# Kernel optimization log

Hardware: AMD Instinct MI355X
Metric: run time of the kernel (lower is better)

Reference implementation:

```python
import jax, jax.numpy as jnp
import numpy as np

B, TT, TA, H = 2, 128, 512, 1024
EPS = 1e-5


def _conv1d(x, w, b, pad):
    # x: [B, C_in, T], w: [C_out, C_in, K] -> [B, C_out, T]
    y = jax.lax.conv_general_dilated(x, w, window_strides=(1,), padding=[(pad, pad)],
                                     dimension_numbers=('NCH', 'OIH', 'NCH'))
    return y + b[None, :, None]


def _groupnorm1(x, g, b):
    # GroupNorm(num_groups=1): normalize over (C, T) per sample. x: [B, C, T]
    mu = jnp.mean(x, axis=(1, 2), keepdims=True)
    var = jnp.var(x, axis=(1, 2), keepdims=True)
    xn = (x - mu) * jax.lax.rsqrt(var + EPS)
    return xn * g[None, :, None] + b[None, :, None]


def setup_inputs() -> dict:
    key = jax.random.key(0)
    ks = jax.random.split(key, 16)
    s = 0.02
    return {
        'text_hidden': jax.random.normal(ks[0], (B, TT, H), jnp.float32),
        'audio_hidden': jax.random.normal(ks[1], (B, TA, H), jnp.float32),
        # alignment_proj: Linear(2H, H) -> ReLU -> Linear(H, 1)
        'a_w1': jax.random.normal(ks[2], (2 * H, H), jnp.float32) * s,
        'a_b1': jnp.zeros((H,), jnp.float32),
        'a_w2': jax.random.normal(ks[3], (H, 1), jnp.float32) * s,
        'a_b2': jnp.zeros((1,), jnp.float32),
        # duration_predictor: Conv1d(H,H,3) ReLU GN(1,H) Conv1d(H,H,3) ReLU GN(1,H) Conv1d(H,1,1)
        'd_w1': jax.random.normal(ks[4], (H, H, 3), jnp.float32) * s,
        'd_b1': jnp.zeros((H,), jnp.float32),
        'gn1_g': jnp.ones((H,), jnp.float32),
        'gn1_b': jnp.zeros((H,), jnp.float32),
        'd_w2': jax.random.normal(ks[5], (H, H, 3), jnp.float32) * s,
        'd_b2': jnp.zeros((H,), jnp.float32),
        'gn2_g': jnp.ones((H,), jnp.float32),
        'gn2_b': jnp.zeros((H,), jnp.float32),
        'd_w3': jax.random.normal(ks[6], (1, H, 1), jnp.float32) * s,
        'd_b3': jnp.zeros((1,), jnp.float32),
    }


def reference(text_hidden, audio_hidden, a_w1, a_b1, a_w2, a_b2,
              d_w1, d_b1, gn1_g, gn1_b, d_w2, d_b2, gn2_g, gn2_b, d_w3, d_b3):
    # ---- predict_durations ----
    x = jnp.swapaxes(text_hidden, 1, 2)                      # [B, H, TT]
    x = _groupnorm1(jax.nn.relu(_conv1d(x, d_w1, d_b1, 1)), gn1_g, gn1_b)
    x = _groupnorm1(jax.nn.relu(_conv1d(x, d_w2, d_b2, 1)), gn2_g, gn2_b)
    x = _conv1d(x, d_w3, d_b3, 0)                            # [B, 1, TT]
    durations = jax.nn.softplus(x[:, 0, :])                  # [B, TT]

    # ---- soft_mas (temperature = 1.0) ----
    # Linear on concat([text, audio]) == text @ W1[:H] + audio @ W1[H:] + b1
    t_part = jnp.einsum('bth,hd->btd', text_hidden, a_w1[:H])    # [B, TT, H]
    a_part = jnp.einsum('bah,hd->bad', audio_hidden, a_w1[H:])   # [B, TA, H]
    hid = jax.nn.relu(t_part[:, :, None, :] + a_part[:, None, :, :] + a_b1)  # [B,TT,TA,H]
    logits = jnp.einsum('btad,do->bta', hid, a_w2) + a_b2[0]     # [B, TT, TA]

    pos = jnp.arange(TA, dtype=logits.dtype)                     # audio positions j
    expected = jnp.arange(TT, dtype=logits.dtype) * (TA / TT)    # expected pos per text i
    monotonic_bias = -0.1 * jnp.abs(pos[None, :] - expected[:, None])  # [TT, TA]
    logits = logits + monotonic_bias[None, :, :]

    alignment = jax.nn.softmax(logits, axis=-1)
    return alignment, durations
```

## Files before the change

kernel.cpp:

```cpp
#include <hip/hip_runtime.h>
#include <hip/hip_bf16.h>


typedef __bf16 bf16_t;
typedef __bf16 bf16x8 __attribute__((ext_vector_type(8)));
typedef __bf16 bf16x4 __attribute__((ext_vector_type(4)));
typedef float  f32x4  __attribute__((ext_vector_type(4)));
typedef _Float16 f16_t;
typedef _Float16 f16x2 __attribute__((ext_vector_type(2)));
typedef _Float16 f16x4 __attribute__((ext_vector_type(4)));
typedef int v4i __attribute__((ext_vector_type(4)));

#define EPSV 1e-5f

#define GLD(dst, ptr, off) \
    asm volatile("global_load_dwordx4 %0, %1, off offset:%c2" \
                 : "=v"(dst) : "v"(ptr), "n"(off) : "memory")
#define WAITV(n) do { \
    asm volatile("s_waitcnt vmcnt(%c0)" :: "n"(n) : "memory"); \
    __builtin_amdgcn_sched_barrier(0); } while (0)

__device__ __forceinline__ bf16x8 as_bf16x8(v4i v) {
    union { v4i i; bf16x8 h; } u; u.i = v; return u.h;
}

#define OFF_TEXTP    0u
#define OFF_AUDIOP   524288u
#define OFF_W1TOP    2621440u
#define OFF_W1BOT    4718592u
#define OFF_WC1      6815744u
#define OFF_WC2      13107200u
#define OFF_TP       19398656u
#define OFF_W2F      19922944u
#define OFF_APT      20447232u
#define OFF_XP0      22544384u
#define OFF_XP1      23076864u
#define OFF_Y2       23609344u
#define OFF_BST1     24133632u
#define OFF_BST2     24137728u
#define OFF_LP       24141824u
#define OFF_SG       26238976u
#define OFF_SB       26251264u
#define OFF_SGF      26263552u
#define OFF_SBF      26267648u

__global__ __launch_bounds__(256) void prep_k(
    const float* __restrict__ text, const float* __restrict__ audio,
    const float* __restrict__ w1,
    const float* __restrict__ w1c, const float* __restrict__ w2c,
    const float* __restrict__ w2,
    const float* __restrict__ g1, const float* __restrict__ b1g,
    bf16_t* __restrict__ textP, bf16_t* __restrict__ xp0,
    bf16_t* __restrict__ audioP,
    bf16_t* __restrict__ topP, bf16_t* __restrict__ botP,
    bf16_t* __restrict__ wc1, bf16_t* __restrict__ wc2,
    bf16_t* __restrict__ xp1, f16_t* __restrict__ w2f,
    float* __restrict__ Sg, float* __restrict__ Sb,
    float* __restrict__ SgF, float* __restrict__ SbF)
{
    __shared__ float tile[32][33];
    const int bid = blockIdx.x;
    if (bid < 1280) {
        const int e = (bid * 256 + threadIdx.x) * 4;
        if (e < 262144) {
            float4 v = *(const float4*)&text[e];
            bf16x4 o; o[0] = (bf16_t)v.x; o[1] = (bf16_t)v.y; o[2] = (bf16_t)v.z; o[3] = (bf16_t)v.w;
            const int bt = e >> 10, h = e & 1023;
            const int b = bt >> 7, t = bt & 127;
            *(bf16x4*)&xp0[(size_t)(b * 130 + 1 + t) * 1024 + h] = o;
            const int lane = (bt & 15) | (((h >> 3) & 3) << 4);
            *(bf16x4*)&textP[((size_t)((bt >> 4) * 32 + (h >> 5))) * 512 + lane * 8 + (h & 7)] = o;
        } else {
            const int ea = e - 262144;
            float4 v = *(const float4*)&audio[ea];
            bf16x4 o; o[0] = (bf16_t)v.x; o[1] = (bf16_t)v.y; o[2] = (bf16_t)v.z; o[3] = (bf16_t)v.w;
            const int ba = ea >> 10, h = ea & 1023;
            const int lane = (ba & 15) | (((h >> 3) & 3) << 4);
            *(bf16x4*)&audioP[((size_t)((ba >> 4) * 32 + (h >> 5))) * 512 + lane * 8 + (h & 7)] = o;
        }
    } else if (bid < 3328) {
        const int b2 = bid - 1280;
        const int bx = b2 & 31, by = b2 >> 5;
        const int tx = threadIdx.x & 31, ty = threadIdx.x >> 5;
        #pragma unroll
        for (int j = 0; j < 4; ++j)
            tile[ty + j * 8][tx] = w1[(size_t)(by * 32 + ty + j * 8) * 1024 + bx * 32 + tx];
        __syncthreads();
        if (threadIdx.x < 128) {
            const int rbl = threadIdx.x >> 6, lane = threadIdx.x & 63;
            const int dl = rbl * 16 + (lane & 15);
            const int lkp = lane >> 4;
            bf16x8 v8;
            #pragma unroll
            for (int e2 = 0; e2 < 8; ++e2) v8[e2] = (bf16_t)tile[lkp * 8 + e2][dl];
            const int d = bx * 32 + dl;
            bf16_t* out = (by < 32) ? topP : botP;
            *(bf16x8*)&out[((size_t)((d >> 4) * 32 + (by & 31))) * 512 + lane * 8] = v8;
        }
    } else if (bid < 5376) {
        int b2 = bid - 3328;
        const int is2 = (b2 >= 1024) ? 1 : 0;
        const float* w = is2 ? w2c : w1c;
        bf16_t* wc = is2 ? wc2 : wc1;
        b2 &= 1023;
        const int o = b2, i4 = threadIdx.x;
        const float* src = w + (size_t)o * 3072 + i4 * 12;
        float4 v0 = *(const float4*)&src[0];
        float4 v1 = *(const float4*)&src[4];
        float4 v2 = *(const float4*)&src[8];
        const float f[12] = {v0.x, v0.y, v0.z, v0.w, v1.x, v1.y, v1.z, v1.w, v2.x, v2.y, v2.z, v2.w};
        float g4[4] = {1.f, 1.f, 1.f, 1.f}, bb4[4] = {0.f, 0.f, 0.f, 0.f};
        if (is2) {
            float4 gv = *(const float4*)&g1[i4 * 4];
            float4 bv = *(const float4*)&b1g[i4 * 4];
            g4[0] = gv.x; g4[1] = gv.y; g4[2] = gv.z; g4[3] = gv.w;
            bb4[0] = bv.x; bb4[1] = bv.y; bb4[2] = bv.z; bb4[3] = bv.w;
        }
        const int i0 = i4 * 4;
        const int lane = (o & 15) | (((i0 >> 3) & 3) << 4);
        float sgr[3] = {0.f, 0.f, 0.f}, sbr[3] = {0.f, 0.f, 0.f};
        #pragma unroll
        for (int r = 0; r < 3; ++r) {
            bf16x4 o4;
            #pragma unroll
            for (int j = 0; j < 4; ++j) {
                const float wv = f[j * 3 + r];
                const float ws = wv * g4[j];
                sgr[r] += ws;
                sbr[r] += wv * bb4[j];
                o4[j] = (bf16_t)(is2 ? ws : wv);
            }
            *(bf16x4*)&wc[((size_t)(r * 2048 + (o >> 4) * 32 + (i0 >> 5))) * 512 + lane * 8 + (i0 & 7)] = o4;
        }
        if (is2) {
            #pragma unroll
            for (int off = 32; off > 0; off >>= 1) {
                #pragma unroll
                for (int r = 0; r < 3; ++r) {
                    sgr[r] += __shfl_xor(sgr[r], off);
                    sbr[r] += __shfl_xor(sbr[r], off);
                }
            }
            float* red = &tile[0][0];
            const int wid = threadIdx.x >> 6, lane2 = threadIdx.x & 63;
            if (lane2 == 0) {
                #pragma unroll
                for (int r = 0; r < 3; ++r) {
                    red[wid * 6 + r] = sgr[r];
                    red[wid * 6 + 3 + r] = sbr[r];
                }
            }
            __syncthreads();
            if (threadIdx.x < 6) {
                const float v = red[threadIdx.x] + red[6 + threadIdx.x]
                              + red[12 + threadIdx.x] + red[18 + threadIdx.x];
                if (threadIdx.x < 3) Sg[o * 3 + threadIdx.x] = v;
                else                 Sb[o * 3 + threadIdx.x - 3] = v;
                red[24 + threadIdx.x] = v;
            }
            __syncthreads();
            if (threadIdx.x == 0)      SgF[o] = red[24] + red[25] + red[26];
            else if (threadIdx.x == 1) SbF[o] = red[27] + red[28] + red[29];
        }
    } else {
        const int tid = threadIdx.x;
        const int rowmap[4] = {0, 129, 130, 259};
        const int f = tid * 16;
        const int r = f >> 10, w = f & 1023;
        bf16x8 z8 = (bf16x8)(bf16_t)0.0f;
        bf16_t* p0 = xp0 + (size_t)rowmap[r] * 1024 + w;
        bf16_t* p1 = xp1 + (size_t)rowmap[r] * 1024 + w;
        *(bf16x8*)p0 = z8; *(bf16x8*)(p0 + 8) = z8;
        *(bf16x8*)p1 = z8; *(bf16x8*)(p1 + 8) = z8;
        float4 wv = *(const float4*)&w2[tid * 4];
        f16x4 wo; wo[0] = (f16_t)wv.x; wo[1] = (f16_t)wv.y; wo[2] = (f16_t)wv.z; wo[3] = (f16_t)wv.w;
        *(f16x4*)&w2f[tid * 4] = wo;
    }
}

__device__ __forceinline__ float wave_red_add(float v) {
    #pragma unroll
    for (int off = 32; off > 0; off >>= 1) v += __shfl_xor(v, off);
    return v;
}

__device__ __forceinline__ void conv_body(
    const bf16_t* __restrict__ WcP, const bf16_t* __restrict__ xp,
    int by, int b, int tbase, int w, int l, bf16_t* Bs, int tid,
    f32x4& acc0, f32x4& acc1)
{
    const int lm = l & 15, lk = (l >> 4) * 8;
    const bf16_t* xrow = xp + (size_t)(b * 130 + tbase) * 1024;
    #pragma unroll 1
    for (int c = 0; c < 4; ++c) {
        __syncthreads();
        for (int idx = tid; idx < 1088; idx += 512) {
            const int row = idx >> 5, col = (idx & 31) * 8;
            *(v4i*)&Bs[row * 264 + col] =
                *(const v4i*)&xrow[(size_t)row * 1024 + c * 256 + col];
        }
        __syncthreads();
        const int kc = c * 8 + w;
        const bf16_t* a0 = WcP + ((size_t)(by * 32 + kc)) * 512 + l * 8;
        v4i A0, A1, A2;
        GLD(A0, a0, 0);
        GLD(A1, a0 + 1048576, 0);
        GLD(A2, a0 + 2097152, 0);
        const int cb = w * 32 + lk;
        bf16x8 b00 = *(const bf16x8*)&Bs[(lm + 0) * 264 + cb];
        bf16x8 b10 = *(const bf16x8*)&Bs[(lm + 16) * 264 + cb];
        bf16x8 b01 = *(const bf16x8*)&Bs[(lm + 1) * 264 + cb];
        bf16x8 b11 = *(const bf16x8*)&Bs[(lm + 17) * 264 + cb];
        bf16x8 b02 = *(const bf16x8*)&Bs[(lm + 2) * 264 + cb];
        bf16x8 b12 = *(const bf16x8*)&Bs[(lm + 18) * 264 + cb];
        WAITV(2);
        acc0 = __builtin_amdgcn_mfma_f32_16x16x32_bf16(as_bf16x8(A0), b00, acc0, 0, 0, 0);
        acc1 = __builtin_amdgcn_mfma_f32_16x16x32_bf16(as_bf16x8(A0), b10, acc1, 0, 0, 0);
        WAITV(1);
        acc0 = __builtin_amdgcn_mfma_f32_16x16x32_bf16(as_bf16x8(A1), b01, acc0, 0, 0, 0);
        acc1 = __builtin_amdgcn_mfma_f32_16x16x32_bf16(as_bf16x8(A1), b11, acc1, 0, 0, 0);
        WAITV(0);
        acc0 = __builtin_amdgcn_mfma_f32_16x16x32_bf16(as_bf16x8(A2), b02, acc0, 0, 0, 0);
        acc1 = __builtin_amdgcn_mfma_f32_16x16x32_bf16(as_bf16x8(A2), b12, acc1, 0, 0, 0);
    }
    __syncthreads();
}

__global__ __launch_bounds__(512) void p2_k(
    const bf16_t* __restrict__ wc1, const bf16_t* __restrict__ xp0,
    const float* __restrict__ d_b1, bf16_t* __restrict__ xp1,
    float* __restrict__ bstat1,
    const bf16_t* __restrict__ textP, const bf16_t* __restrict__ topP,
    const float* __restrict__ a_b1, f16_t* __restrict__ tp,
    const bf16_t* __restrict__ audioP, const bf16_t* __restrict__ botP,
    f16_t* __restrict__ apT4)
{
    __shared__ float smem[8448];
    __shared__ float sred[8], sredq[8];
    const int bid = blockIdx.x;
    const int tid = threadIdx.x;
    const int w = tid >> 6, l = tid & 63;
    const int lm = l & 15, lh = l >> 4;
    if (bid < 512) {
        const int bx = bid >> 6, by = bid & 63;
        const int bt0 = bx * 32, m0 = by * 16;
        const int b = bt0 >> 7, tbase = bt0 & 127;
        f32x4 acc0 = (f32x4)(0.0f), acc1 = (f32x4)(0.0f);
        conv_body(wc1, xp0, by, b, tbase, w, l, (bf16_t*)smem, tid, acc0, acc1);
        float* sl = smem + w * 528;
        #pragma unroll
        for (int r = 0; r < 4; ++r) {
            sl[(lh * 4 + r) * 33 + lm] = acc0[r];
            sl[(lh * 4 + r) * 33 + 16 + lm] = acc1[r];
        }
        __syncthreads();
        const int mm = tid >> 5, nn = tid & 31;
        float v = 0.f;
        #pragma unroll
        for (int ww = 0; ww < 8; ++ww) v += smem[ww * 528 + mm * 33 + nn];
        v = fmaxf(v + d_b1[m0 + mm], 0.f);
        float s = wave_red_add(v), q = wave_red_add(v * v);
        if (l == 0) { sred[w] = s; sredq[w] = q; }
        xp1[(size_t)(b * 130 + 1 + tbase + nn) * 1024 + m0 + mm] = (bf16_t)v;
        __syncthreads();
        if (tid == 0) {
            float ts = 0.f, tq = 0.f;
            #pragma unroll
            for (int ww = 0; ww < 8; ++ww) { ts += sred[ww]; tq += sredq[ww]; }
            bstat1[bid * 2] = ts; bstat1[bid * 2 + 1] = tq;
        }
    } else {
        const bf16_t *At, *Bm;
        int d0, r0, is_tp;
        if (bid < 768) {
            const int unit = bid - 512;
            d0 = (unit & 31) * 32; r0 = (unit >> 5) * 32;
            At = topP; Bm = textP; is_tp = 1;
        } else {
            const int unit = bid - 768;
            d0 = (unit & 31) * 32; r0 = (unit >> 5) * 32;
            At = botP; Bm = audioP; is_tp = 0;
        }
        const int rb0 = d0 >> 4, rbB = r0 >> 4;
        const bf16_t* Ap0 = At + ((size_t)(rb0 * 32 + w * 4)) * 512 + l * 8;
        const bf16_t* Ap1 = Ap0 + 16384;
        const bf16_t* Bp0 = Bm + ((size_t)(rbB * 32 + w * 4)) * 512 + l * 8;
        const bf16_t* Bp1 = Bp0 + 16384;
        v4i qa0[4], qa1[4], qb0[4], qb1[4];
        GLD(qa0[0], Ap0,    0); GLD(qa1[0], Ap1,    0); GLD(qb0[0], Bp0,    0); GLD(qb1[0], Bp1,    0);
        GLD(qa0[1], Ap0, 1024); GLD(qa1[1], Ap1, 1024); GLD(qb0[1], Bp0, 1024); GLD(qb1[1], Bp1, 1024);
        GLD(qa0[2], Ap0, 2048); GLD(qa1[2], Ap1, 2048); GLD(qb0[2], Bp0, 2048); GLD(qb1[2], Bp1, 2048);
        GLD(qa0[3], Ap0, 3072); GLD(qa1[3], Ap1, 3072); GLD(qb0[3], Bp0, 3072); GLD(qb1[3], Bp1, 3072);
        f32x4 acc[2][2];
        #pragma unroll
        for (int mt = 0; mt < 2; ++mt)
            #pragma unroll
            for (int nt = 0; nt < 2; ++nt) acc[mt][nt] = (f32x4)(0.0f);
#define GMF(cc, n) \
        WAITV(n); \
        acc[0][0] = __builtin_amdgcn_mfma_f32_16x16x32_bf16(as_bf16x8(qa0[cc]), as_bf16x8(qb0[cc]), acc[0][0], 0, 0, 0); \
        acc[0][1] = __builtin_amdgcn_mfma_f32_16x16x32_bf16(as_bf16x8(qa0[cc]), as_bf16x8(qb1[cc]), acc[0][1], 0, 0, 0); \
        acc[1][0] = __builtin_amdgcn_mfma_f32_16x16x32_bf16(as_bf16x8(qa1[cc]), as_bf16x8(qb0[cc]), acc[1][0], 0, 0, 0); \
        acc[1][1] = __builtin_amdgcn_mfma_f32_16x16x32_bf16(as_bf16x8(qa1[cc]), as_bf16x8(qb1[cc]), acc[1][1], 0, 0, 0)
        GMF(0, 12); GMF(1, 8); GMF(2, 4); GMF(3, 0);
#undef GMF
        float* sl = smem + w * 1056;
        #pragma unroll
        for (int mt = 0; mt < 2; ++mt)
            #pragma unroll
            for (int nt = 0; nt < 2; ++nt)
                #pragma unroll
                for (int r = 0; r < 4; ++r)
                    sl[(mt * 16 + lh * 4 + r) * 33 + nt * 16 + lm] = acc[mt][nt][r];
        __syncthreads();
        const int m = tid >> 4, n2 = (tid & 15) * 2;
        float v0 = 0.f, v1 = 0.f;
        #pragma unroll
        for (int ww = 0; ww < 8; ++ww) {
            v0 += smem[ww * 1056 + m * 33 + n2];
            v1 += smem[ww * 1056 + m * 33 + n2 + 1];
        }
        if (is_tp) {
            const float bb = a_b1[d0 + m];
            tp[(size_t)(r0 + n2) * 1024 + d0 + m] = (f16_t)(v0 + bb);
            tp[(size_t)(r0 + n2 + 1) * 1024 + d0 + m] = (f16_t)(v1 + bb);
        } else {
            const int h = d0 + m, hq = h >> 2, hr = h & 3;
            const int a0 = r0 + n2;
            const int bbk = a0 >> 9, al = a0 & 511;
            apT4[((size_t)hq * 1024 + bbk * 512 + al) * 4 + hr] = (f16_t)v0;
            apT4[((size_t)hq * 1024 + bbk * 512 + al + 1) * 4 + hr] = (f16_t)v1;
        }
    }
}

__device__ __forceinline__ void reduce_bstat(
    const float* __restrict__ bstat, int b, int tid,
    float* sr, float* sq, float& mu, float& rsig)
{
    const int lane = tid & 63, wid = tid >> 6;
    float s = 0.f, q = 0.f;
    if (tid < 256) {
        float2 v = ((const float2*)bstat)[b * 256 + tid];
        s = v.x; q = v.y;
    }
    #pragma unroll
    for (int off = 32; off > 0; off >>= 1) {
        s += __shfl_xor(s, off);
        q += __shfl_xor(q, off);
    }
    if (lane == 0) { sr[wid] = s; sq[wid] = q; }
    __syncthreads();
    float ts = 0.f, tq = 0.f;
    #pragma unroll
    for (int i = 0; i < 8; ++i) { ts += sr[i]; tq += sq[i]; }
    const float cnt = 131072.f;
    mu = ts / cnt;
    const float var = tq / cnt - mu * mu;
    rsig = rsqrtf(var + EPSV);
}

__device__ __forceinline__ float dot2_acc(f16x2 x, f16x2 w, float acc) {
#if __has_builtin(__builtin_amdgcn_fdot2)
    return __builtin_amdgcn_fdot2(x, w, acc, false);
#else
    return acc + (float)x[0] * (float)w[0] + (float)x[1] * (float)w[1];
#endif
}

__global__ __launch_bounds__(512) void p3_k(
    const bf16_t* __restrict__ wc2, const bf16_t* __restrict__ xp1,
    const float* __restrict__ d_b2, bf16_t* __restrict__ y2,
    float* __restrict__ bstat2, const float* __restrict__ bstat1,
    const float* __restrict__ SgF, const float* __restrict__ SbF,
    const float* __restrict__ Sg3, const float* __restrict__ Sb3,
    const f16_t* __restrict__ tp, const f16_t* __restrict__ apT4,
    const f16_t* __restrict__ w2f, float* __restrict__ lp)
{
    __shared__ float smem[4608];
    __shared__ float sred[8], sredq[8], sr[8], sq[8];
    const int bid = blockIdx.x;
    const int tid = threadIdx.x;
    if (bid < 512) {
        const int w = tid >> 6, l = tid & 63;
        const int lm = l & 15, lh = l >> 4;
        const int bx = bid >> 6, by = bid & 63;
        const int bt0 = bx * 32, m0 = by * 16;
        const int b = bt0 >> 7, tbase = bt0 & 127;
        f32x4 acc0 = (f32x4)(0.0f), acc1 = (f32x4)(0.0f);
        conv_body(wc2, xp1, by, b, tbase, w, l, (bf16_t*)smem, tid, acc0, acc1);
        float* sl = smem + w * 528;
        #pragma unroll
        for (int r = 0; r < 4; ++r) {
            sl[(lh * 4 + r) * 33 + lm] = acc0[r];
            sl[(lh * 4 + r) * 33 + 16 + lm] = acc1[r];
        }
        __syncthreads();
        const int mm = tid >> 5, nn = tid & 31;
        float vraw = 0.f;
        #pragma unroll
        for (int ww = 0; ww < 8; ++ww) vraw += smem[ww * 528 + mm * 33 + nn];
        float mu, rsig;
        reduce_bstat(bstat1, b, tid, sr, sq, mu, rsig);
        const int o = m0 + mm, tloc = tbase + nn;
        float sg = SgF[o], sb = SbF[o];
        if (tloc == 0)   { sg -= Sg3[o * 3];     sb -= Sb3[o * 3]; }
        if (tloc == 127) { sg -= Sg3[o * 3 + 2]; sb -= Sb3[o * 3 + 2]; }
        float v = fmaxf(rsig * vraw + sb - mu * rsig * sg + d_b2[o], 0.f);
        float s = wave_red_add(v), q = wave_red_add(v * v);
        if ((tid & 63) == 0) { sred[tid >> 6] = s; sredq[tid >> 6] = q; }
        y2[(size_t)(b * 128 + tloc) * 1024 + o] = (bf16_t)v;
        __syncthreads();
        if (tid == 0) {
            float ts = 0.f, tq = 0.f;
            #pragma unroll
            for (int ww = 0; ww < 8; ++ww) { ts += sred[ww]; tq += sredq[ww]; }
            bstat2[bid * 2] = ts; bstat2[bid * 2 + 1] = tq;
        }
    } else {
        const int lb = bid - 512;
        const int hc = lb >> 6, btp = lb & 63;
        const int bt0 = btp * 4;
        const int b = bt0 >> 7;
        const int a = tid;
        const f16_t* tpr = tp + (size_t)bt0 * 1024 + hc * 256;
        const f16_t* w2r = w2f + hc * 256;
        const f16_t* apc = apT4 + ((size_t)(hc * 64) * 1024 + b * 512 + a) * 4;
        float acc[4] = {0.f, 0.f, 0.f, 0.f};
        const f16x2 zero = (f16x2)(f16_t)0.0f;
#define L_A0(i) (*(const f16x4*)(apc + (size_t)(2 * (i)) * 4096))
#define L_A1(i) (*(const f16x4*)(apc + (size_t)(2 * (i) + 1) * 4096))
        constexpr int PF = 4;
        f16x4 pa[PF], pb[PF];
        #pragma unroll
        for (int i = 0; i < PF; ++i) { pa[i] = L_A0(i); pb[i] = L_A1(i); }
        #pragma unroll
        for (int i = 0; i < 32; ++i) {
            const int sl = i % PF;
            const int hq = 2 * i;
            f16x4 a0 = pa[sl], a1 = pb[sl];
            f16x4 w0 = *(const f16x4*)&w2r[hq * 4];
            f16x4 w1 = *(const f16x4*)&w2r[hq * 4 + 4];
            #pragma unroll
            for (int r = 0; r < 4; ++r) {
                f16x4 t0 = *(const f16x4*)&tpr[r * 1024 + hq * 4];
                f16x4 t1 = *(const f16x4*)&tpr[r * 1024 + hq * 4 + 4];
                f16x2 p;
                p = __builtin_elementwise_max((f16x2){t0[0] + a0[0], t0[1] + a0[1]}, zero);
                acc[r] = dot2_acc(p, (f16x2){w0[0], w0[1]}, acc[r]);
                p = __builtin_elementwise_max((f16x2){t0[2] + a0[2], t0[3] + a0[3]}, zero);
                acc[r] = dot2_acc(p, (f16x2){w0[2], w0[3]}, acc[r]);
                p = __builtin_elementwise_max((f16x2){t1[0] + a1[0], t1[1] + a1[1]}, zero);
                acc[r] = dot2_acc(p, (f16x2){w1[0], w1[1]}, acc[r]);
                p = __builtin_elementwise_max((f16x2){t1[2] + a1[2], t1[3] + a1[3]}, zero);
                acc[r] = dot2_acc(p, (f16x2){w1[2], w1[3]}, acc[r]);
            }
            const int nx = i + PF;
            if (nx < 32) { pa[sl] = L_A0(nx); pb[sl] = L_A1(nx); }
        }
#undef L_A0
#undef L_A1
        float* dst = lp + (size_t)(hc * 256 + bt0) * 512 + a;
        #pragma unroll
        for (int r = 0; r < 4; ++r) dst[(size_t)r * 512] = acc[r];
    }
}

__global__ __launch_bounds__(512) void combine_k(
    const float* __restrict__ lp, const float* __restrict__ b2,
    const bf16_t* __restrict__ y2, const float* __restrict__ bstat2,
    const float* __restrict__ g, const float* __restrict__ bet,
    const float* __restrict__ w3, const float* __restrict__ b3,
    float* __restrict__ out)
{
    __shared__ float redm[8], redsum[8];
    const int bid = blockIdx.x;
    const int tid = threadIdx.x;
    if (bid < 256) {
        const int bt = bid, t = bt & 127;
        const int a = tid;
        const int lane = a & 63, wid = a >> 6;
        const size_t base = (size_t)bt * 512 + a;
        float v = lp[base] + lp[131072 + base] + lp[262144 + base] + lp[393216 + base];
        v += b2[0] - 0.1f * fabsf((float)a - 4.0f * (float)t);
        float m = v;
        #pragma unroll
        for (int off = 32; off > 0; off >>= 1) m = fmaxf(m, __shfl_xor(m, off));
        if (lane == 0) redm[wid] = m;
        __syncthreads();
        float M = redm[0];
        #pragma unroll
        for (int i = 1; i < 8; ++i) M = fmaxf(M, redm[i]);
        const float e = expf(v - M);
        float s = e;
        #pragma unroll
        for (int off = 32; off > 0; off >>= 1) s += __shfl_xor(s, off);
        if (lane == 0) redsum[wid] = s;
        __syncthreads();
        float S = redsum[0];
        #pragma unroll
        for (int i = 1; i < 8; ++i) S += redsum[i];
        out[(size_t)bt * 512 + a] = e * (1.0f / S);
    } else {
        const int cb = bid - 256;
        const int b = (cb * 8) >> 7;
        float mu, rsig;
        reduce_bstat(bstat2, b, tid, redm, redsum, mu, rsig);
        const int lane = tid & 63, w = tid >> 6;
        const int bt = cb * 8 + w;
        const bf16_t* row = y2 + (size_t)bt * 1024 + lane * 16;
        float s1 = 0.f, s2 = 0.f, s3 = 0.f;
        #pragma unroll
        for (int c = 0; c < 2; ++c) {
            bf16x8 yv = *(const bf16x8*)(row + c * 8);
            #pragma unroll
            for (int j = 0; j < 8; ++j) {
                const int i = lane * 16 + c * 8 + j;
                const float gw = g[i] * w3[i];
                s1 += gw * (float)yv[j];
                s2 += gw;
                s3 += bet[i] * w3[i];
            }
        }
        #pragma unroll
        for (int off = 32; off > 0; off >>= 1) {
            s1 += __shfl_xor(s1, off);
            s2 += __shfl_xor(s2, off);
            s3 += __shfl_xor(s3, off);
        }
        if (lane == 0) {
            const float t = rsig * (s1 - mu * s2) + s3 + b3[0];
            out[131072 + bt] = fmaxf(t, 0.f) + log1pf(expf(-fabsf(t)));
        }
    }
}

extern "C" void kernel_launch(void* const* d_in, const int* in_sizes, int n_in,
                              void* d_out, int out_size, void* d_ws, size_t ws_size,
                              hipStream_t stream) {
    const float* text   = (const float*)d_in[0];
    const float* audio  = (const float*)d_in[1];
    const float* a_w1   = (const float*)d_in[2];
    const float* a_b1   = (const float*)d_in[3];
    const float* a_w2   = (const float*)d_in[4];
    const float* a_b2   = (const float*)d_in[5];
    const float* d_w1   = (const float*)d_in[6];
    const float* d_b1   = (const float*)d_in[7];
    const float* gn1_g  = (const float*)d_in[8];
    const float* gn1_b  = (const float*)d_in[9];
    const float* d_w2   = (const float*)d_in[10];
    const float* d_b2   = (const float*)d_in[11];
    const float* gn2_g  = (const float*)d_in[12];
    const float* gn2_b  = (const float*)d_in[13];
    const float* d_w3   = (const float*)d_in[14];
    const float* d_b3   = (const float*)d_in[15];

    char* ws = (char*)d_ws;
    float* outf = (float*)d_out;

    bf16_t* textP    = (bf16_t*)(ws + OFF_TEXTP);
    bf16_t* audioP   = (bf16_t*)(ws + OFF_AUDIOP);
    bf16_t* topP     = (bf16_t*)(ws + OFF_W1TOP);
    bf16_t* botP     = (bf16_t*)(ws + OFF_W1BOT);
    bf16_t* wc1      = (bf16_t*)(ws + OFF_WC1);
    bf16_t* wc2      = (bf16_t*)(ws + OFF_WC2);
    f16_t*  tp       = (f16_t*) (ws + OFF_TP);
    f16_t*  w2f      = (f16_t*) (ws + OFF_W2F);
    f16_t*  apT4     = (f16_t*) (ws + OFF_APT);
    bf16_t* xp0      = (bf16_t*)(ws + OFF_XP0);
    bf16_t* xp1      = (bf16_t*)(ws + OFF_XP1);
    bf16_t* y2       = (bf16_t*)(ws + OFF_Y2);
    float*  bstat1   = (float*) (ws + OFF_BST1);
    float*  bstat2   = (float*) (ws + OFF_BST2);
    float*  lp       = (float*) (ws + OFF_LP);
    float*  Sg3      = (float*) (ws + OFF_SG);
    float*  Sb3      = (float*) (ws + OFF_SB);
    float*  SgFp     = (float*) (ws + OFF_SGF);
    float*  SbFp     = (float*) (ws + OFF_SBF);

    prep_k<<<dim3(5377), 256, 0, stream>>>(text, audio, a_w1, d_w1, d_w2, a_w2,
                                           gn1_g, gn1_b,
                                           textP, xp0, audioP, topP, botP,
                                           wc1, wc2, xp1, w2f, Sg3, Sb3,
                                           SgFp, SbFp);
    p2_k<<<dim3(1792), 512, 0, stream>>>(wc1, xp0, d_b1, xp1, bstat1,
                                         textP, topP, a_b1, tp,
                                         audioP, botP, apT4);
    p3_k<<<dim3(768), 512, 0, stream>>>(wc2, xp1, d_b2, y2, bstat2, bstat1,
                                        SgFp, SbFp, Sg3, Sb3, tp, apT4, w2f, lp);
    combine_k<<<dim3(288), 512, 0, stream>>>(lp, a_b2, y2, bstat2,
                                             gn2_g, gn2_b, d_w3, d_b3, outf);
}
```

Before: 152.8 us.

## Move conv2 weight prep into p2 kernel, pair stores, prefetch A before LDS fill

The conv2 weight repacking and GroupNorm-folding sums move out of the prep kernel into extra blocks of the second kernel, so this work runs alongside the conv1 and projection GEMMs and the prep kernel shrinks. Packed bf16 stores are merged into 16-byte writes by exchanging halves between adjacent lanes. In the conv loop, the global A-fragment loads are now issued before the shared-memory tile fill, which hides their latency. The trade-off is a larger p2 grid, where the extra blocks compete with the GEMM blocks for compute units.

```diff
diff --git a/kernel.cpp b/kernel.cpp
--- a/kernel.cpp
+++ b/kernel.cpp
@@ -22,6 +22,17 @@
 
 __device__ __forceinline__ bf16x8 as_bf16x8(v4i v) {
     union { v4i i; bf16x8 h; } u; u.i = v; return u.h;
+}
+
+__device__ __forceinline__ void pair_store16(bf16_t* even_addr, bf16x4 v, int t) {
+    union { bf16x4 h; unsigned u[2]; } a; a.h = v;
+    const unsigned ox = __shfl_down(a.u[0], 1);
+    const unsigned oy = __shfl_down(a.u[1], 1);
+    if (!(t & 1)) {
+        union { unsigned u[4]; v4i i; } o;
+        o.u[0] = a.u[0]; o.u[1] = a.u[1]; o.u[2] = ox; o.u[3] = oy;
+        *(v4i*)even_addr = o.i;
+    }
 }
 
 #define OFF_TEXTP    0u
@@ -47,47 +58,48 @@
 __global__ __launch_bounds__(256) void prep_k(
     const float* __restrict__ text, const float* __restrict__ audio,
     const float* __restrict__ w1,
-    const float* __restrict__ w1c, const float* __restrict__ w2c,
-    const float* __restrict__ w2,
-    const float* __restrict__ g1, const float* __restrict__ b1g,
+    const float* __restrict__ w1c, const float* __restrict__ w2,
     bf16_t* __restrict__ textP, bf16_t* __restrict__ xp0,
     bf16_t* __restrict__ audioP,
     bf16_t* __restrict__ topP, bf16_t* __restrict__ botP,
-    bf16_t* __restrict__ wc1, bf16_t* __restrict__ wc2,
-    bf16_t* __restrict__ xp1, f16_t* __restrict__ w2f,
-    float* __restrict__ Sg, float* __restrict__ Sb,
-    float* __restrict__ SgF, float* __restrict__ SbF)
+    bf16_t* __restrict__ wc1,
+    bf16_t* __restrict__ xp1, f16_t* __restrict__ w2f)
 {
     __shared__ float tile[32][33];
     const int bid = blockIdx.x;
+    const int tid = threadIdx.x;
     if (bid < 1280) {
-        const int e = (bid * 256 + threadIdx.x) * 4;
+        const int e = (bid * 256 + tid) * 4;
         if (e < 262144) {
             float4 v = *(const float4*)&text[e];
             bf16x4 o; o[0] = (bf16_t)v.x; o[1] = (bf16_t)v.y; o[2] = (bf16_t)v.z; o[3] = (bf16_t)v.w;
             const int bt = e >> 10, h = e & 1023;
             const int b = bt >> 7, t = bt & 127;
             *(bf16x4*)&xp0[(size_t)(b * 130 + 1 + t) * 1024 + h] = o;
-            const int lane = (bt & 15) | (((h >> 3) & 3) << 4);
-            *(bf16x4*)&textP[((size_t)((bt >> 4) * 32 + (h >> 5))) * 512 + lane * 8 + (h & 7)] = o;
+            const int h0 = h & ~7;
+            const int lane = (bt & 15) | (((h0 >> 3) & 3) << 4);
+            bf16_t* ea = &textP[((size_t)((bt >> 4) * 32 + (h0 >> 5))) * 512 + lane * 8];
+            pair_store16(ea, o, tid);
         } else {
-            const int ea = e - 262144;
-            float4 v = *(const float4*)&audio[ea];
+            const int ea4 = e - 262144;
+            float4 v = *(const float4*)&audio[ea4];
             bf16x4 o; o[0] = (bf16_t)v.x; o[1] = (bf16_t)v.y; o[2] = (bf16_t)v.z; o[3] = (bf16_t)v.w;
-            const int ba = ea >> 10, h = ea & 1023;
-            const int lane = (ba & 15) | (((h >> 3) & 3) << 4);
-            *(bf16x4*)&audioP[((size_t)((ba >> 4) * 32 + (h >> 5))) * 512 + lane * 8 + (h & 7)] = o;
+            const int ba = ea4 >> 10, h = ea4 & 1023;
+            const int h0 = h & ~7;
+            const int lane = (ba & 15) | (((h0 >> 3) & 3) << 4);
+            bf16_t* ea = &audioP[((size_t)((ba >> 4) * 32 + (h0 >> 5))) * 512 + lane * 8];
+            pair_store16(ea, o, tid);
         }
     } else if (bid < 3328) {
         const int b2 = bid - 1280;
         const int bx = b2 & 31, by = b2 >> 5;
-        const int tx = threadIdx.x & 31, ty = threadIdx.x >> 5;
+        const int tx = tid & 31, ty = tid >> 5;
         #pragma unroll
         for (int j = 0; j < 4; ++j)
             tile[ty + j * 8][tx] = w1[(size_t)(by * 32 + ty + j * 8) * 1024 + bx * 32 + tx];
         __syncthreads();
-        if (threadIdx.x < 128) {
-            const int rbl = threadIdx.x >> 6, lane = threadIdx.x & 63;
+        if (tid < 128) {
+            const int rbl = tid >> 6, lane = tid & 63;
             const int dl = rbl * 16 + (lane & 15);
             const int lkp = lane >> 4;
             bf16x8 v8;
@@ -97,73 +109,25 @@
             bf16_t* out = (by < 32) ? topP : botP;
             *(bf16x8*)&out[((size_t)((d >> 4) * 32 + (by & 31))) * 512 + lane * 8] = v8;
         }
-    } else if (bid < 5376) {
-        int b2 = bid - 3328;
-        const int is2 = (b2 >= 1024) ? 1 : 0;
-        const float* w = is2 ? w2c : w1c;
-        bf16_t* wc = is2 ? wc2 : wc1;
-        b2 &= 1023;
-        const int o = b2, i4 = threadIdx.x;
-        const float* src = w + (size_t)o * 3072 + i4 * 12;
+    } else if (bid < 4352) {
+        const int o = bid - 3328;
+        const int i0 = tid * 4;
+        const float* src = w1c + (size_t)o * 3072 + tid * 12;
         float4 v0 = *(const float4*)&src[0];
         float4 v1 = *(const float4*)&src[4];
         float4 v2 = *(const float4*)&src[8];
         const float f[12] = {v0.x, v0.y, v0.z, v0.w, v1.x, v1.y, v1.z, v1.w, v2.x, v2.y, v2.z, v2.w};
-        float g4[4] = {1.f, 1.f, 1.f, 1.f}, bb4[4] = {0.f, 0.f, 0.f, 0.f};
-        if (is2) {
-            float4 gv = *(const float4*)&g1[i4 * 4];
-            float4 bv = *(const float4*)&b1g[i4 * 4];
-            g4[0] = gv.x; g4[1] = gv.y; g4[2] = gv.z; g4[3] = gv.w;
-            bb4[0] = bv.x; bb4[1] = bv.y; bb4[2] = bv.z; bb4[3] = bv.w;
-        }
-        const int i0 = i4 * 4;
-        const int lane = (o & 15) | (((i0 >> 3) & 3) << 4);
-        float sgr[3] = {0.f, 0.f, 0.f}, sbr[3] = {0.f, 0.f, 0.f};
+        const int ip = i0 & ~7;
+        const int lane = (o & 15) | (((ip >> 3) & 3) << 4);
         #pragma unroll
         for (int r = 0; r < 3; ++r) {
             bf16x4 o4;
             #pragma unroll
-            for (int j = 0; j < 4; ++j) {
-                const float wv = f[j * 3 + r];
-                const float ws = wv * g4[j];
-                sgr[r] += ws;
-                sbr[r] += wv * bb4[j];
-                o4[j] = (bf16_t)(is2 ? ws : wv);
-            }
-            *(bf16x4*)&wc[((size_t)(r * 2048 + (o >> 4) * 32 + (i0 >> 5))) * 512 + lane * 8 + (i0 & 7)] = o4;
-        }
-        if (is2) {
-            #pragma unroll
-            for (int off = 32; off > 0; off >>= 1) {
-                #pragma unroll
-                for (int r = 0; r < 3; ++r) {
-                    sgr[r] += __shfl_xor(sgr[r], off);
-                    sbr[r] += __shfl_xor(sbr[r], off);
-                }
-            }
-            float* red = &tile[0][0];
-            const int wid = threadIdx.x >> 6, lane2 = threadIdx.x & 63;
-            if (lane2 == 0) {
-                #pragma unroll
-                for (int r = 0; r < 3; ++r) {
-                    red[wid * 6 + r] = sgr[r];
-                    red[wid * 6 + 3 + r] = sbr[r];
-                }
-            }
-            __syncthreads();
-            if (threadIdx.x < 6) {
-                const float v = red[threadIdx.x] + red[6 + threadIdx.x]
-                              + red[12 + threadIdx.x] + red[18 + threadIdx.x];
-                if (threadIdx.x < 3) Sg[o * 3 + threadIdx.x] = v;
-                else                 Sb[o * 3 + threadIdx.x - 3] = v;
-                red[24 + threadIdx.x] = v;
-            }
-            __syncthreads();
-            if (threadIdx.x == 0)      SgF[o] = red[24] + red[25] + red[26];
-            else if (threadIdx.x == 1) SbF[o] = red[27] + red[28] + red[29];
+            for (int j = 0; j < 4; ++j) o4[j] = (bf16_t)f[j * 3 + r];
+            bf16_t* ea = &wc1[((size_t)(r * 2048 + (o >> 4) * 32 + (ip >> 5))) * 512 + lane * 8];
+            pair_store16(ea, o4, tid);
         }
     } else {
-        const int tid = threadIdx.x;
         const int rowmap[4] = {0, 129, 130, 259};
         const int f = tid * 16;
         const int r = f >> 10, w = f & 1023;
@@ -194,18 +158,18 @@
     #pragma unroll 1
     for (int c = 0; c < 4; ++c) {
         __syncthreads();
-        for (int idx = tid; idx < 1088; idx += 512) {
-            const int row = idx >> 5, col = (idx & 31) * 8;
-            *(v4i*)&Bs[row * 264 + col] =
-                *(const v4i*)&xrow[(size_t)row * 1024 + c * 256 + col];
-        }
-        __syncthreads();
         const int kc = c * 8 + w;
         const bf16_t* a0 = WcP + ((size_t)(by * 32 + kc)) * 512 + l * 8;
         v4i A0, A1, A2;
         GLD(A0, a0, 0);
         GLD(A1, a0 + 1048576, 0);
         GLD(A2, a0 + 2097152, 0);
+        for (int idx = tid; idx < 1088; idx += 512) {
+            const int row = idx >> 5, col = (idx & 31) * 8;
+            *(v4i*)&Bs[row * 264 + col] =
+                *(const v4i*)&xrow[(size_t)row * 1024 + c * 256 + col];
+        }
+        __syncthreads();
         const int cb = w * 32 + lk;
         bf16x8 b00 = *(const bf16x8*)&Bs[(lm + 0) * 264 + cb];
         bf16x8 b10 = *(const bf16x8*)&Bs[(lm + 16) * 264 + cb];
@@ -233,7 +197,11 @@
     const bf16_t* __restrict__ textP, const bf16_t* __restrict__ topP,
     const float* __restrict__ a_b1, f16_t* __restrict__ tp,
     const bf16_t* __restrict__ audioP, const bf16_t* __restrict__ botP,
-    f16_t* __restrict__ apT4)
+    f16_t* __restrict__ apT4,
+    const float* __restrict__ w2c, const float* __restrict__ g1,
+    const float* __restrict__ b1g, bf16_t* __restrict__ wc2,
+    float* __restrict__ Sg3, float* __restrict__ Sb3,
+    float* __restrict__ SgF, float* __restrict__ SbF)
 {
     __shared__ float smem[8448];
     __shared__ float sred[8], sredq[8];
@@ -269,7 +237,7 @@
             for (int ww = 0; ww < 8; ++ww) { ts += sred[ww]; tq += sredq[ww]; }
             bstat1[bid * 2] = ts; bstat1[bid * 2 + 1] = tq;
         }
-    } else {
+    } else if (bid < 1792) {
         const bf16_t *At, *Bm;
         int d0, r0, is_tp;
         if (bid < 768) {
@@ -331,6 +299,63 @@
             apT4[((size_t)hq * 1024 + bbk * 512 + al) * 4 + hr] = (f16_t)v0;
             apT4[((size_t)hq * 1024 + bbk * 512 + al + 1) * 4 + hr] = (f16_t)v1;
         }
+    } else {
+        const int half = tid >> 8, t = tid & 255;
+        const int o = (bid - 1792) * 2 + half;
+        const int i0 = t * 4;
+        const float* src = w2c + (size_t)o * 3072 + t * 12;
+        float4 v0 = *(const float4*)&src[0];
+        float4 v1 = *(const float4*)&src[4];
+        float4 v2 = *(const float4*)&src[8];
+        const float f[12] = {v0.x, v0.y, v0.z, v0.w, v1.x, v1.y, v1.z, v1.w, v2.x, v2.y, v2.z, v2.w};
+        float4 gv = *(const float4*)&g1[i0];
+        float4 bv = *(const float4*)&b1g[i0];
+        const float g4[4] = {gv.x, gv.y, gv.z, gv.w};
+        const float bb4[4] = {bv.x, bv.y, bv.z, bv.w};
+        const int ip = i0 & ~7;
+        const int lane = (o & 15) | (((ip >> 3) & 3) << 4);
+        float sgr[3] = {0.f, 0.f, 0.f}, sbr[3] = {0.f, 0.f, 0.f};
+        #pragma unroll
+        for (int r = 0; r < 3; ++r) {
+            bf16x4 o4;
+            #pragma unroll
+            for (int j = 0; j < 4; ++j) {
+                const float wv = f[j * 3 + r];
+                const float ws = wv * g4[j];
+                sgr[r] += ws;
+                sbr[r] += wv * bb4[j];
+                o4[j] = (bf16_t)ws;
+            }
+            bf16_t* ea = &wc2[((size_t)(r * 2048 + (o >> 4) * 32 + (ip >> 5))) * 512 + lane * 8];
+            pair_store16(ea, o4, t);
+        }
+        #pragma unroll
+        for (int off = 32; off > 0; off >>= 1) {
+            #pragma unroll
+            for (int r = 0; r < 3; ++r) {
+                sgr[r] += __shfl_xor(sgr[r], off);
+                sbr[r] += __shfl_xor(sbr[r], off);
+            }
+        }
+        float* red = smem + half * 32;
+        const int wid = t >> 6, lane2 = t & 63;
+        if (lane2 == 0) {
+            #pragma unroll
+            for (int r = 0; r < 3; ++r) {
+                red[wid * 6 + r] = sgr[r];
+                red[wid * 6 + 3 + r] = sbr[r];
+            }
+        }
+        __syncthreads();
+        if (t < 6) {
+            const float v = red[t] + red[6 + t] + red[12 + t] + red[18 + t];
+            if (t < 3) Sg3[o * 3 + t] = v;
+            else       Sb3[o * 3 + t - 3] = v;
+            red[24 + t] = v;
+        }
+        __syncthreads();
+        if (t == 0)      SgF[o] = red[24] + red[25] + red[26];
+        else if (t == 1) SbF[o] = red[27] + red[28] + red[29];
     }
 }
 
@@ -578,14 +603,14 @@
     float*  SgFp     = (float*) (ws + OFF_SGF);
     float*  SbFp     = (float*) (ws + OFF_SBF);
 
-    prep_k<<<dim3(5377), 256, 0, stream>>>(text, audio, a_w1, d_w1, d_w2, a_w2,
-                                           gn1_g, gn1_b,
+    prep_k<<<dim3(4353), 256, 0, stream>>>(text, audio, a_w1, d_w1, a_w2,
                                            textP, xp0, audioP, topP, botP,
-                                           wc1, wc2, xp1, w2f, Sg3, Sb3,
-                                           SgFp, SbFp);
-    p2_k<<<dim3(1792), 512, 0, stream>>>(wc1, xp0, d_b1, xp1, bstat1,
+                                           wc1, xp1, w2f);
+    p2_k<<<dim3(2304), 512, 0, stream>>>(wc1, xp0, d_b1, xp1, bstat1,
                                          textP, topP, a_b1, tp,
-                                         audioP, botP, apT4);
+                                         audioP, botP, apT4,
+                                         d_w2, gn1_g, gn1_b, wc2,
+                                         Sg3, Sb3, SgFp, SbFp);
     p3_k<<<dim3(768), 512, 0, stream>>>(wc2, xp1, d_b2, y2, bstat2, bstat1,
                                         SgFp, SbFp, Sg3, Sb3, tp, apT4, w2f, lp);
     combine_k<<<dim3(288), 512, 0, stream>>>(lp, a_b2, y2, bstat2,
```

Result: no change. 150.7 us, median of 2 (-1.3%).
